# Kernel tuning notes

Measured on AMD Instinct MI355X. Metric: run time of the kernel, lower is better.

The kernel has to match this reference:

```python
import jax, jax.numpy as jnp
import numpy as np

N_NODES = 50000
HEADS = 4
OUT_DIM = 64
NEG_SLOPE = 0.2
BETA = 0.5
C_CONST = 1.0
EPS = 1e-16


def setup_inputs() -> dict:
    key = jax.random.key(0)
    ks = jax.random.split(key, 6)
    in_dim = 128
    x = jax.random.normal(ks[0], (N_NODES, in_dim), dtype=jnp.float32)
    edge_index = jax.random.randint(ks[1], (2, 800000), 0, N_NODES, dtype=jnp.int64)
    # GATConv params (glorot-ish scale)
    W = jax.random.normal(ks[2], (in_dim, HEADS * OUT_DIM), dtype=jnp.float32) * (1.0 / np.sqrt(in_dim))
    att_src = jax.random.normal(ks[3], (HEADS, OUT_DIM), dtype=jnp.float32) * (1.0 / np.sqrt(OUT_DIM))
    att_dst = jax.random.normal(ks[4], (HEADS, OUT_DIM), dtype=jnp.float32) * (1.0 / np.sqrt(OUT_DIM))
    bias = jnp.zeros((HEADS * OUT_DIM,), dtype=jnp.float32)
    return {"x": x, "edge_index": edge_index, "W": W, "att_src": att_src,
            "att_dst": att_dst, "bias": bias}


def _gat_conv(x, edge_index, W, att_src, att_dst, bias):
    N = x.shape[0]
    # add self loops (PyG GATConv default)
    loop = jnp.arange(N, dtype=edge_index.dtype)
    src = jnp.concatenate([edge_index[0], loop])
    dst = jnp.concatenate([edge_index[1], loop])
    # linear transform: [N, H, F]
    h = (x @ W).reshape(N, HEADS, OUT_DIM)
    # per-node attention logits: [N, H]
    a_src = jnp.einsum('nhf,hf->nh', h, att_src)
    a_dst = jnp.einsum('nhf,hf->nh', h, att_dst)
    # per-edge logits and segment softmax over destination nodes
    e = jax.nn.leaky_relu(a_src[src] + a_dst[dst], negative_slope=NEG_SLOPE)  # [E, H]
    m = jax.ops.segment_max(e, dst, num_segments=N)                           # [N, H]
    ex = jnp.exp(e - m[dst])
    s = jax.ops.segment_sum(ex, dst, num_segments=N)                          # [N, H]
    alpha = ex / (s[dst] + EPS)                                               # [E, H]
    # aggregate messages: [N, H, F]
    out = jax.ops.segment_sum(alpha[:, :, None] * h[src], dst, num_segments=N)
    return out.reshape(N, HEADS * OUT_DIM) + bias


def reference(x, edge_index, W, att_src, att_dst, bias):
    # eval mode: feature dropout and attention dropout are identity
    z = _gat_conv(x, edge_index, W, att_src, att_dst, bias)
    return BETA * z + (C_CONST - BETA) * jax.nn.elu(z)
```

## Files before the change

### kernel.cpp

```cpp
#include <hip/hip_runtime.h>
#include <hip/hip_bf16.h>

typedef unsigned short u16;
typedef __attribute__((ext_vector_type(8))) short bf16x8;
typedef __attribute__((ext_vector_type(4))) float f32x4;

#define HEADS 4
#define OUT_DIM 64
#define HF 256
#define IN_DIM 128
#define NEG_SLOPE 0.2f
#define EPSF 1e-16f

__device__ __forceinline__ float braw2f(u16 u) {
    union { float f; unsigned int i; } c; c.i = ((unsigned int)u) << 16; return c.f;
}
__device__ __forceinline__ u16 f2braw(float v) {
    __hip_bfloat16 t = __float2bfloat16(v);
    return *(u16*)&t;
}
__device__ __forceinline__ float lrelu(float e) { return e < 0.f ? NEG_SLOPE * e : e; }

__device__ __forceinline__ bool detect_i64(const int* ei) {
    return (ei[1] | ei[3] | ei[5] | ei[7] | ei[9] | ei[11] | ei[13] | ei[15]) == 0;
}
__device__ __forceinline__ void get_edge(const int* ei, int E, int t, bool i64,
                                         int& s, int& d) {
    if (t < E) {
        if (i64) { s = ei[2 * t]; d = ei[2 * (E + t)]; }
        else     { s = ei[t];     d = ei[E + t]; }
    } else {
        s = d = t - E;
    }
}

__global__ __launch_bounds__(256) void init_kernel(const float* __restrict__ W,
                                                   const float* __restrict__ att_s,
                                                   const float* __restrict__ att_d,
                                                   float* __restrict__ wa_s,
                                                   float* __restrict__ wa_d,
                                                   int* __restrict__ cnt, int N, int NZ) {
    int b = blockIdx.x;
    if (b < NZ) {
        int i = b * 256 + threadIdx.x;
        if (i < N) cnt[i] = 0;
    } else {
        for (int idx = threadIdx.x; idx < HEADS * IN_DIM; idx += 256) {
            int h = idx >> 7, k = idx & 127;
            float ss = 0.f, sd = 0.f;
            for (int f = 0; f < OUT_DIM; ++f) {
                float wv = W[k * HF + h * OUT_DIM + f];
                ss = fmaf(wv, att_s[h * OUT_DIM + f], ss);
                sd = fmaf(wv, att_d[h * OUT_DIM + f], sd);
            }
            wa_s[idx] = ss;
            wa_d[idx] = sd;
        }
    }
}

__global__ __launch_bounds__(256) void phase1_kernel(const float* __restrict__ x,
                                                     const int* __restrict__ ei,
                                                     const float* __restrict__ W,
                                                     const float* __restrict__ wa_s,
                                                     const float* __restrict__ wa_d,
                                                     float* __restrict__ a_src,
                                                     float* __restrict__ a_dst,
                                                     u16* __restrict__ xb,
                                                     u16* __restrict__ Wfrag,
                                                     int* __restrict__ cnt,
                                                     int N, int E, int NA, int NC) {
    int b = blockIdx.x;
    if (b < NA) {
        int v = (b * 256 + threadIdx.x) >> 6;
        int l = threadIdx.x & 63;
        if (v >= N) return;
        int h = l >> 4, c = l & 15, kc = c * 8;

        const float4* xr = (const float4*)(x + (size_t)v * IN_DIM + kc);
        float4 x0 = xr[0], x1 = xr[1];
        const float4* s4 = (const float4*)(wa_s + h * IN_DIM + kc);
        const float4* d4 = (const float4*)(wa_d + h * IN_DIM + kc);
        float4 s0 = s4[0], s1 = s4[1], d0 = d4[0], d1 = d4[1];

        float ps = x0.x*s0.x + x0.y*s0.y + x0.z*s0.z + x0.w*s0.w
                 + x1.x*s1.x + x1.y*s1.y + x1.z*s1.z + x1.w*s1.w;
        float pd = x0.x*d0.x + x0.y*d0.y + x0.z*d0.z + x0.w*d0.w
                 + x1.x*d1.x + x1.y*d1.y + x1.z*d1.z + x1.w*d1.w;
        #pragma unroll
        for (int off = 1; off < 16; off <<= 1) {
            ps += __shfl_xor(ps, off);
            pd += __shfl_xor(pd, off);
        }
        if (c == 0) {
            a_src[v * HEADS + h] = ps;
            a_dst[v * HEADS + h] = pd;
        }
        if (h == 0) {
            uint4 u;
            u.x = (unsigned)f2braw(x0.x) | ((unsigned)f2braw(x0.y) << 16);
            u.y = (unsigned)f2braw(x0.z) | ((unsigned)f2braw(x0.w) << 16);
            u.z = (unsigned)f2braw(x1.x) | ((unsigned)f2braw(x1.y) << 16);
            u.w = (unsigned)f2braw(x1.z) | ((unsigned)f2braw(x1.w) << 16);
            *(uint4*)(xb + (size_t)v * IN_DIM + kc) = u;
        }
    } else if (b < NA + NC) {
        int t = (b - NA) * 256 + threadIdx.x;
        if (t >= E + N) return;
        bool i64 = detect_i64(ei);
        int src, dst; get_edge(ei, E, t, i64, src, dst);
        if (src >= 0 && src < N && dst >= 0 && dst < N) atomicAdd(cnt + dst, 1);
    } else {
        int bb = b - NA - NC;
        for (int idx = bb * 256 + threadIdx.x; idx < 32768; idx += 8 * 256) {
            int j = idx & 7, l = (idx >> 3) & 63, t = (idx >> 9) & 3;
            int s = (idx >> 11) & 3, h = (idx >> 13) & 3;
            int k = s * 32 + ((l >> 4) & 3) * 8 + j;
            int col = h * OUT_DIM + t * 16 + (l & 15);
            Wfrag[idx] = f2braw(W[k * HF + col]);
        }
    }
}

__global__ __launch_bounds__(256) void scan1_kernel(const int* __restrict__ cnt,
                                                    int* __restrict__ indptr,
                                                    int* __restrict__ bsum, int N) {
    __shared__ int sc[256];
    int tid = threadIdx.x;
    int idx = blockIdx.x * 256 + tid;
    int v = (idx < N) ? cnt[idx] : 0;
    sc[tid] = v;
    __syncthreads();
    #pragma unroll
    for (int off = 1; off < 256; off <<= 1) {
        int t = (tid >= off) ? sc[tid - off] : 0;
        __syncthreads();
        sc[tid] += t;
        __syncthreads();
    }
    if (idx < N) indptr[idx + 1] = sc[tid];
    if (tid == 255) bsum[blockIdx.x] = sc[255];
}

__global__ __launch_bounds__(1024) void scan2_kernel(int* __restrict__ bsum, int T) {
    __shared__ int sc[1024];
    int tid = threadIdx.x;
    int v = (tid < T) ? bsum[tid] : 0;
    sc[tid] = v;
    __syncthreads();
    #pragma unroll
    for (int off = 1; off < 1024; off <<= 1) {
        int t = (tid >= off) ? sc[tid - off] : 0;
        __syncthreads();
        sc[tid] += t;
        __syncthreads();
    }
    if (tid < T) bsum[tid] = sc[tid] - v;
}

__global__ __launch_bounds__(256) void scan3_kernel(int* __restrict__ indptr,
                                                    const int* __restrict__ bsum,
                                                    int* __restrict__ cnt, int N) {
    int idx = blockIdx.x * 256 + threadIdx.x;
    if (idx < N) {
        indptr[idx + 1] += bsum[blockIdx.x];
        cnt[idx] = 0;
    }
    if (idx == 0) indptr[0] = 0;
}

__global__ __launch_bounds__(256) void fill_kernel(const int* __restrict__ ei,
                                                   const int* __restrict__ indptr,
                                                   int* __restrict__ cur,
                                                   int* __restrict__ slots,
                                                   uint2* __restrict__ wslots,
                                                   const float* __restrict__ a_src,
                                                   const float* __restrict__ a_dst,
                                                   int E, int N) {
    int t = blockIdx.x * 256 + threadIdx.x;
    if (t >= E + N) return;
    bool i64 = detect_i64(ei);
    int src, dst; get_edge(ei, E, t, i64, src, dst);
    if (src >= 0 && src < N && dst >= 0 && dst < N) {
        int pos = atomicAdd(cur + dst, 1);
        int idx = indptr[dst] + pos;
        slots[idx] = src;
        if (wslots) {
            float4 as = ((const float4*)a_src)[src];
            float4 ad = ((const float4*)a_dst)[dst];
            float w0 = __expf(lrelu(as.x + ad.x));
            float w1 = __expf(lrelu(as.y + ad.y));
            float w2 = __expf(lrelu(as.z + ad.z));
            float w3 = __expf(lrelu(as.w + ad.w));
            uint2 wp;
            wp.x = (unsigned)f2braw(w0) | ((unsigned)f2braw(w1) << 16);
            wp.y = (unsigned)f2braw(w2) | ((unsigned)f2braw(w3) << 16);
            wslots[idx] = wp;
        }
    }
}

__global__ __launch_bounds__(512) void gather_w_kernel(const int* __restrict__ indptr,
                                                       const int* __restrict__ slots,
                                                       const uint2* __restrict__ wslots,
                                                       const u16* __restrict__ xb,
                                                       u16* __restrict__ Gout, int N, int ET) {
    int l = threadIdx.x & 63;
    int gw = blockIdx.x * 8 + (threadIdx.x >> 6);
    int v = gw * 4 + (l >> 4);
    if (v >= N) return;
    int c = l & 15, kc = c * 8;

    int beg = indptr[v], end = indptr[v + 1];
    beg = max(0, min(beg, ET));
    end = max(beg, min(end, ET));

    float ls0 = 0.f, ls1 = 0.f, ls2 = 0.f, ls3 = 0.f;
    float G0[8] = {0,0,0,0,0,0,0,0};
    float G1[8] = {0,0,0,0,0,0,0,0};
    float G2[8] = {0,0,0,0,0,0,0,0};
    float G3[8] = {0,0,0,0,0,0,0,0};

    int j = beg;
    for (; j + 2 <= end; j += 2) {
        int s0 = max(0, min(slots[j],     N - 1));
        int s1 = max(0, min(slots[j + 1], N - 1));
        uint2 wp0 = wslots[j];
        uint2 wp1 = wslots[j + 1];
        uint4 r0 = *(const uint4*)(xb + (size_t)s0 * IN_DIM + kc);
        uint4 r1 = *(const uint4*)(xb + (size_t)s1 * IN_DIM + kc);

        float a0 = braw2f(wp0.x & 0xffff), a1 = braw2f(wp0.x >> 16);
        float a2 = braw2f(wp0.y & 0xffff), a3 = braw2f(wp0.y >> 16);
        ls0 += a0; ls1 += a1; ls2 += a2; ls3 += a3;
        {
            float xv[8];
            xv[0] = braw2f(r0.x & 0xffff); xv[1] = braw2f(r0.x >> 16);
            xv[2] = braw2f(r0.y & 0xffff); xv[3] = braw2f(r0.y >> 16);
            xv[4] = braw2f(r0.z & 0xffff); xv[5] = braw2f(r0.z >> 16);
            xv[6] = braw2f(r0.w & 0xffff); xv[7] = braw2f(r0.w >> 16);
            #pragma unroll
            for (int q = 0; q < 8; ++q) {
                G0[q] = fmaf(a0, xv[q], G0[q]);
                G1[q] = fmaf(a1, xv[q], G1[q]);
                G2[q] = fmaf(a2, xv[q], G2[q]);
                G3[q] = fmaf(a3, xv[q], G3[q]);
            }
        }
        float b0 = braw2f(wp1.x & 0xffff), b1 = braw2f(wp1.x >> 16);
        float b2 = braw2f(wp1.y & 0xffff), b3 = braw2f(wp1.y >> 16);
        ls0 += b0; ls1 += b1; ls2 += b2; ls3 += b3;
        {
            float xv[8];
            xv[0] = braw2f(r1.x & 0xffff); xv[1] = braw2f(r1.x >> 16);
            xv[2] = braw2f(r1.y & 0xffff); xv[3] = braw2f(r1.y >> 16);
            xv[4] = braw2f(r1.z & 0xffff); xv[5] = braw2f(r1.z >> 16);
            xv[6] = braw2f(r1.w & 0xffff); xv[7] = braw2f(r1.w >> 16);
            #pragma unroll
            for (int q = 0; q < 8; ++q) {
                G0[q] = fmaf(b0, xv[q], G0[q]);
                G1[q] = fmaf(b1, xv[q], G1[q]);
                G2[q] = fmaf(b2, xv[q], G2[q]);
                G3[q] = fmaf(b3, xv[q], G3[q]);
            }
        }
    }
    if (j < end) {
        int s0 = max(0, min(slots[j], N - 1));
        uint2 wp0 = wslots[j];
        uint4 r0 = *(const uint4*)(xb + (size_t)s0 * IN_DIM + kc);
        float a0 = braw2f(wp0.x & 0xffff), a1 = braw2f(wp0.x >> 16);
        float a2 = braw2f(wp0.y & 0xffff), a3 = braw2f(wp0.y >> 16);
        ls0 += a0; ls1 += a1; ls2 += a2; ls3 += a3;
        float xv[8];
        xv[0] = braw2f(r0.x & 0xffff); xv[1] = braw2f(r0.x >> 16);
        xv[2] = braw2f(r0.y & 0xffff); xv[3] = braw2f(r0.y >> 16);
        xv[4] = braw2f(r0.z & 0xffff); xv[5] = braw2f(r0.z >> 16);
        xv[6] = braw2f(r0.w & 0xffff); xv[7] = braw2f(r0.w >> 16);
        #pragma unroll
        for (int q = 0; q < 8; ++q) {
            G0[q] = fmaf(a0, xv[q], G0[q]);
            G1[q] = fmaf(a1, xv[q], G1[q]);
            G2[q] = fmaf(a2, xv[q], G2[q]);
            G3[q] = fmaf(a3, xv[q], G3[q]);
        }
    }

    float i0 = 1.f / (ls0 + EPSF), i1 = 1.f / (ls1 + EPSF);
    float i2 = 1.f / (ls2 + EPSF), i3 = 1.f / (ls3 + EPSF);
    u16* gout = Gout + (size_t)v * 512 + kc;
    #pragma unroll
    for (int h = 0; h < 4; ++h) {
        const float* G = h == 0 ? G0 : h == 1 ? G1 : h == 2 ? G2 : G3;
        float inv = h == 0 ? i0 : h == 1 ? i1 : h == 2 ? i2 : i3;
        uint4 u;
        u.x = (unsigned)f2braw(G[0] * inv) | ((unsigned)f2braw(G[1] * inv) << 16);
        u.y = (unsigned)f2braw(G[2] * inv) | ((unsigned)f2braw(G[3] * inv) << 16);
        u.z = (unsigned)f2braw(G[4] * inv) | ((unsigned)f2braw(G[5] * inv) << 16);
        u.w = (unsigned)f2braw(G[6] * inv) | ((unsigned)f2braw(G[7] * inv) << 16);
        *(uint4*)(gout + h * 128) = u;
    }
}

__global__ __launch_bounds__(512) void gather_bf_kernel(const int* __restrict__ indptr,
                                                        const int* __restrict__ slots,
                                                        const u16* __restrict__ xb,
                                                        const float* __restrict__ a_src,
                                                        const float* __restrict__ a_dst,
                                                        u16* __restrict__ Gout, int N, int ET) {
    int v = (blockIdx.x * 512 + threadIdx.x) >> 6;
    int l = threadIdx.x & 63;
    if (v >= N) return;
    int h = l >> 4, c = l & 15, kc = c * 8;

    int beg = indptr[v], end = indptr[v + 1];
    beg = max(0, min(beg, ET));
    end = max(beg, min(end, ET));
    float adh = a_dst[v * HEADS + h];

    float ls = 0.f;
    float G[8] = {0.f,0.f,0.f,0.f,0.f,0.f,0.f,0.f};

    int j = beg;
    for (; j + 4 <= end; j += 4) {
        int s0 = max(0, min(slots[j],     N - 1));
        int s1 = max(0, min(slots[j + 1], N - 1));
        int s2 = max(0, min(slots[j + 2], N - 1));
        int s3 = max(0, min(slots[j + 3], N - 1));
        float w0 = __expf(lrelu(a_src[s0 * HEADS + h] + adh));
        float w1 = __expf(lrelu(a_src[s1 * HEADS + h] + adh));
        float w2 = __expf(lrelu(a_src[s2 * HEADS + h] + adh));
        float w3 = __expf(lrelu(a_src[s3 * HEADS + h] + adh));
        uint4 r0 = *(const uint4*)(xb + (size_t)s0 * IN_DIM + kc);
        uint4 r1 = *(const uint4*)(xb + (size_t)s1 * IN_DIM + kc);
        uint4 r2 = *(const uint4*)(xb + (size_t)s2 * IN_DIM + kc);
        uint4 r3 = *(const uint4*)(xb + (size_t)s3 * IN_DIM + kc);
        ls += (w0 + w1) + (w2 + w3);
        unsigned ua[4];
        ua[0]=r0.x; ua[1]=r0.y; ua[2]=r0.z; ua[3]=r0.w;
        #pragma unroll
        for (int q = 0; q < 4; ++q) {
            G[2*q]   = fmaf(w0, braw2f(ua[q] & 0xffff), G[2*q]);
            G[2*q+1] = fmaf(w0, braw2f(ua[q] >> 16),    G[2*q+1]);
        }
        ua[0]=r1.x; ua[1]=r1.y; ua[2]=r1.z; ua[3]=r1.w;
        #pragma unroll
        for (int q = 0; q < 4; ++q) {
            G[2*q]   = fmaf(w1, braw2f(ua[q] & 0xffff), G[2*q]);
            G[2*q+1] = fmaf(w1, braw2f(ua[q] >> 16),    G[2*q+1]);
        }
        ua[0]=r2.x; ua[1]=r2.y; ua[2]=r2.z; ua[3]=r2.w;
        #pragma unroll
        for (int q = 0; q < 4; ++q) {
            G[2*q]   = fmaf(w2, braw2f(ua[q] & 0xffff), G[2*q]);
            G[2*q+1] = fmaf(w2, braw2f(ua[q] >> 16),    G[2*q+1]);
        }
        ua[0]=r3.x; ua[1]=r3.y; ua[2]=r3.z; ua[3]=r3.w;
        #pragma unroll
        for (int q = 0; q < 4; ++q) {
            G[2*q]   = fmaf(w3, braw2f(ua[q] & 0xffff), G[2*q]);
            G[2*q+1] = fmaf(w3, braw2f(ua[q] >> 16),    G[2*q+1]);
        }
    }
    for (; j < end; ++j) {
        int s0 = max(0, min(slots[j], N - 1));
        float w0 = __expf(lrelu(a_src[s0 * HEADS + h] + adh));
        uint4 r0 = *(const uint4*)(xb + (size_t)s0 * IN_DIM + kc);
        ls += w0;
        unsigned ua[4]; ua[0]=r0.x; ua[1]=r0.y; ua[2]=r0.z; ua[3]=r0.w;
        #pragma unroll
        for (int q = 0; q < 4; ++q) {
            G[2*q]   = fmaf(w0, braw2f(ua[q] & 0xffff), G[2*q]);
            G[2*q+1] = fmaf(w0, braw2f(ua[q] >> 16),    G[2*q+1]);
        }
    }

    float inv = 1.f / (ls + EPSF);
    uint4 u;
    u.x = (unsigned)f2braw(G[0] * inv) | ((unsigned)f2braw(G[1] * inv) << 16);
    u.y = (unsigned)f2braw(G[2] * inv) | ((unsigned)f2braw(G[3] * inv) << 16);
    u.z = (unsigned)f2braw(G[4] * inv) | ((unsigned)f2braw(G[5] * inv) << 16);
    u.w = (unsigned)f2braw(G[6] * inv) | ((unsigned)f2braw(G[7] * inv) << 16);
    *(uint4*)(Gout + (size_t)v * 512 + h * 128 + kc) = u;
}

__global__ __launch_bounds__(512) void gather_f32_kernel(const int* __restrict__ indptr,
                                                         const int* __restrict__ slots,
                                                         const float* __restrict__ x,
                                                         const float* __restrict__ a_src,
                                                         const float* __restrict__ a_dst,
                                                         u16* __restrict__ Gout, int N, int ET) {
    int v = (blockIdx.x * 512 + threadIdx.x) >> 6;
    int l = threadIdx.x & 63;
    if (v >= N) return;
    int h = l >> 4, c = l & 15, kc = c * 8;

    int beg = indptr[v], end = indptr[v + 1];
    beg = max(0, min(beg, ET));
    end = max(beg, min(end, ET));
    float adh = a_dst[v * HEADS + h];

    float ls = 0.f;
    float G[8] = {0.f,0.f,0.f,0.f,0.f,0.f,0.f,0.f};
    for (int j = beg; j < end; ++j) {
        int s0 = max(0, min(slots[j], N - 1));
        float w0 = __expf(lrelu(a_src[s0 * HEADS + h] + adh));
        const float4* xr0 = (const float4*)(x + (size_t)s0 * IN_DIM + kc);
        float4 a0 = xr0[0], b0 = xr0[1];
        ls += w0;
        G[0]=fmaf(w0,a0.x,G[0]); G[1]=fmaf(w0,a0.y,G[1]);
        G[2]=fmaf(w0,a0.z,G[2]); G[3]=fmaf(w0,a0.w,G[3]);
        G[4]=fmaf(w0,b0.x,G[4]); G[5]=fmaf(w0,b0.y,G[5]);
        G[6]=fmaf(w0,b0.z,G[6]); G[7]=fmaf(w0,b0.w,G[7]);
    }
    float inv = 1.f / (ls + EPSF);
    uint4 u;
    u.x = (unsigned)f2braw(G[0] * inv) | ((unsigned)f2braw(G[1] * inv) << 16);
    u.y = (unsigned)f2braw(G[2] * inv) | ((unsigned)f2braw(G[3] * inv) << 16);
    u.z = (unsigned)f2braw(G[4] * inv) | ((unsigned)f2braw(G[5] * inv) << 16);
    u.w = (unsigned)f2braw(G[6] * inv) | ((unsigned)f2braw(G[7] * inv) << 16);
    *(uint4*)(Gout + (size_t)v * 512 + h * 128 + kc) = u;
}

__global__ __launch_bounds__(256) void zgemm_kernel(const u16* __restrict__ Wfrag,
                                                    const float* __restrict__ bias,
                                                    float* __restrict__ out, int N) {
    int h = threadIdx.x >> 6;
    int l = threadIdx.x & 63;
    int q = l >> 4, mcol = l & 15;
    int nb = blockIdx.x * 16;

    const u16* G = (const u16*)out;
    bool valid = (nb + mcol) < N;
    int vA = valid ? nb + mcol : N - 1;
    const u16* gp = G + (size_t)vA * 512 + h * 128 + q * 8;
    bf16x8 A[4];
    A[0] = *(const bf16x8*)(gp);
    A[1] = *(const bf16x8*)(gp + 32);
    A[2] = *(const bf16x8*)(gp + 64);
    A[3] = *(const bf16x8*)(gp + 96);
    if (!valid) {
        bf16x8 zz = {0,0,0,0,0,0,0,0};
        A[0] = zz; A[1] = zz; A[2] = zz; A[3] = zz;
    }

    f32x4 acc0 = {0.f,0.f,0.f,0.f}, acc1 = acc0, acc2 = acc0, acc3 = acc0;
    #pragma unroll
    for (int s = 0; s < 4; ++s) {
        const u16* wb = Wfrag + (((h * 4 + s) * 4) << 9) + l * 8;
        bf16x8 B0 = *(const bf16x8*)(wb);
        bf16x8 B1 = *(const bf16x8*)(wb + 512);
        bf16x8 B2 = *(const bf16x8*)(wb + 1024);
        bf16x8 B3 = *(const bf16x8*)(wb + 1536);
        acc0 = __builtin_amdgcn_mfma_f32_16x16x32_bf16(A[s], B0, acc0, 0, 0, 0);
        acc1 = __builtin_amdgcn_mfma_f32_16x16x32_bf16(A[s], B1, acc1, 0, 0, 0);
        acc2 = __builtin_amdgcn_mfma_f32_16x16x32_bf16(A[s], B2, acc2, 0, 0, 0);
        acc3 = __builtin_amdgcn_mfma_f32_16x16x32_bf16(A[s], B3, acc3, 0, 0, 0);
    }

    #pragma unroll
    for (int t = 0; t < 4; ++t) {
        f32x4 a = t == 0 ? acc0 : t == 1 ? acc1 : t == 2 ? acc2 : acc3;
        float b = bias[h * OUT_DIM + t * 16 + mcol];
        #pragma unroll
        for (int r = 0; r < 4; ++r) {
            int v = nb + q * 4 + r;
            if (v < N) {
                float z = a[r] + b;
                float y = z > 0.f ? z : 0.5f * z + 0.5f * (__expf(z) - 1.f);
                out[(size_t)v * HF + h * OUT_DIM + t * 16 + mcol] = y;
            }
        }
    }
}

extern "C" void kernel_launch(void* const* d_in, const int* in_sizes, int n_in,
                              void* d_out, int out_size, void* d_ws, size_t ws_size,
                              hipStream_t stream) {
    const float* x       = (const float*)d_in[0];
    const int*   ei      = (const int*)d_in[1];
    const float* W       = (const float*)d_in[2];
    const float* att_src = (const float*)d_in[3];
    const float* att_dst = (const float*)d_in[4];
    const float* bias    = (const float*)d_in[5];

    const int N = in_sizes[0] / IN_DIM;
    const int E = in_sizes[1] / 2;
    const int ET = E + N;
    const int NT = (N + 255) / 256;

    char* ws = (char*)d_ws;
    size_t off = 0;
    float* wa_s   = (float*)(ws + off); off += HEADS * IN_DIM * 4;
    float* wa_d   = (float*)(ws + off); off += HEADS * IN_DIM * 4;
    u16*   Wfrag  = (u16*)(ws + off);   off += 32768 * 2;
    float* a_src  = (float*)(ws + off); off += (size_t)N * HEADS * 4;
    float* a_dst  = (float*)(ws + off); off += (size_t)N * HEADS * 4;
    int*   indptr = (int*)(ws + off);   off += ((size_t)(N + 1) * 4 + 15) & ~(size_t)15;
    int*   cnt    = (int*)(ws + off);   off += ((size_t)N * 4 + 15) & ~(size_t)15;
    int*   bsum   = (int*)(ws + off);   off += 1024 * 4;
    int*   slots  = (int*)(ws + off);   off += ((size_t)ET * 4 + 15) & ~(size_t)15;
    u16*   xb     = (u16*)(ws + off);   size_t need_bf = off + (size_t)N * IN_DIM * 2;
    uint2* wslots = (uint2*)(ws + need_bf);
    size_t need_w = need_bf + (size_t)ET * 8;
    bool use_bf = (ws_size >= need_bf);
    bool use_w  = (ws_size >= need_w);

    const int NA = (N + 3) / 4;
    const int NC = (ET + 255) / 256;

    init_kernel<<<NT + 1, 256, 0, stream>>>(W, att_src, att_dst, wa_s, wa_d, cnt, N, NT);
    phase1_kernel<<<NA + NC + 8, 256, 0, stream>>>(x, ei, W, wa_s, wa_d, a_src, a_dst,
                                                   use_bf ? xb : (u16*)d_out,
                                                   Wfrag, cnt, N, E, NA, NC);
    scan1_kernel<<<NT, 256, 0, stream>>>(cnt, indptr, bsum, N);
    scan2_kernel<<<1, 1024, 0, stream>>>(bsum, NT);
    scan3_kernel<<<NT, 256, 0, stream>>>(indptr, bsum, cnt, N);
    fill_kernel<<<(ET + 255) / 256, 256, 0, stream>>>(ei, indptr, cnt, slots,
                                                      use_w ? wslots : (uint2*)0,
                                                      a_src, a_dst, E, N);
    if (use_w) {
        int nwaves = (N + 3) / 4;
        gather_w_kernel<<<(nwaves * 64 + 511) / 512, 512, 0, stream>>>(indptr, slots,
                                                                       wslots, xb,
                                                                       (u16*)d_out, N, ET);
    } else if (use_bf) {
        gather_bf_kernel<<<(N * 64 + 511) / 512, 512, 0, stream>>>(indptr, slots, xb,
                                                                   a_src, a_dst,
                                                                   (u16*)d_out, N, ET);
    } else {
        gather_f32_kernel<<<(N * 64 + 511) / 512, 512, 0, stream>>>(indptr, slots, x,
                                                                    a_src, a_dst,
                                                                    (u16*)d_out, N, ET);
    }
    zgemm_kernel<<<(N + 15) / 16, 256, 0, stream>>>(Wfrag, bias, (float*)d_out, N);
}
```

Measured before the change: 267.3 us.

## Replace three-kernel prefix scan with atomic wave-level offset allocation

Swaps the scan1/scan2/scan3 exclusive scan for a single kernel. Each wave does a shuffle scan of in-degrees and reserves a contiguous slot range with one atomicAdd on a global counter. The gather kernels now read the offset and degree instead of indptr[v], indptr[v+1], and a separate cur array is zeroed in init, which removes two kernel launches and their dependency chain. The phase1 node path is also reworked so each 16-lane group handles one node across all four heads, cutting redundant x loads and writing a_src/a_dst as float4; the cost is that CSR segments are no longer stored in node order.

```diff
diff --git a/kernel.cpp b/kernel.cpp
--- a/kernel.cpp
+++ b/kernel.cpp
@@ -39,11 +39,15 @@
                                                    const float* __restrict__ att_d,
                                                    float* __restrict__ wa_s,
                                                    float* __restrict__ wa_d,
-                                                   int* __restrict__ cnt, int N, int NZ) {
+                                                   int* __restrict__ cnt,
+                                                   int* __restrict__ cur,
+                                                   int* __restrict__ gcnt,
+                                                   int N, int NZ) {
     int b = blockIdx.x;
+    if (b == 0 && threadIdx.x == 0) *gcnt = 0;
     if (b < NZ) {
         int i = b * 256 + threadIdx.x;
-        if (i < N) cnt[i] = 0;
+        if (i < N) { cnt[i] = 0; cur[i] = 0; }
     } else {
         for (int idx = threadIdx.x; idx < HEADS * IN_DIM; idx += 256) {
             int h = idx >> 7, k = idx & 127;
@@ -72,37 +76,47 @@
                                                      int N, int E, int NA, int NC) {
     int b = blockIdx.x;
     if (b < NA) {
-        int v = (b * 256 + threadIdx.x) >> 6;
+        int wid = threadIdx.x >> 6;
         int l = threadIdx.x & 63;
+        int g = l >> 4, c = l & 15, kc = c * 8;
+        int v = b * 16 + wid * 4 + g;
         if (v >= N) return;
-        int h = l >> 4, c = l & 15, kc = c * 8;
 
         const float4* xr = (const float4*)(x + (size_t)v * IN_DIM + kc);
         float4 x0 = xr[0], x1 = xr[1];
-        const float4* s4 = (const float4*)(wa_s + h * IN_DIM + kc);
-        const float4* d4 = (const float4*)(wa_d + h * IN_DIM + kc);
-        float4 s0 = s4[0], s1 = s4[1], d0 = d4[0], d1 = d4[1];
-
-        float ps = x0.x*s0.x + x0.y*s0.y + x0.z*s0.z + x0.w*s0.w
-                 + x1.x*s1.x + x1.y*s1.y + x1.z*s1.z + x1.w*s1.w;
-        float pd = x0.x*d0.x + x0.y*d0.y + x0.z*d0.z + x0.w*d0.w
-                 + x1.x*d1.x + x1.y*d1.y + x1.z*d1.z + x1.w*d1.w;
+
+        uint4 u;
+        u.x = (unsigned)f2braw(x0.x) | ((unsigned)f2braw(x0.y) << 16);
+        u.y = (unsigned)f2braw(x0.z) | ((unsigned)f2braw(x0.w) << 16);
+        u.z = (unsigned)f2braw(x1.x) | ((unsigned)f2braw(x1.y) << 16);
+        u.w = (unsigned)f2braw(x1.z) | ((unsigned)f2braw(x1.w) << 16);
+        *(uint4*)(xb + (size_t)v * IN_DIM + kc) = u;
+
+        float ps[4], pd[4];
+        #pragma unroll
+        for (int h = 0; h < 4; ++h) {
+            const float4* s4 = (const float4*)(wa_s + h * IN_DIM + kc);
+            const float4* d4 = (const float4*)(wa_d + h * IN_DIM + kc);
+            float4 s0 = s4[0], s1 = s4[1], d0 = d4[0], d1 = d4[1];
+            ps[h] = x0.x*s0.x + x0.y*s0.y + x0.z*s0.z + x0.w*s0.w
+                  + x1.x*s1.x + x1.y*s1.y + x1.z*s1.z + x1.w*s1.w;
+            pd[h] = x0.x*d0.x + x0.y*d0.y + x0.z*d0.z + x0.w*d0.w
+                  + x1.x*d1.x + x1.y*d1.y + x1.z*d1.z + x1.w*d1.w;
+        }
         #pragma unroll
         for (int off = 1; off < 16; off <<= 1) {
-            ps += __shfl_xor(ps, off);
-            pd += __shfl_xor(pd, off);
+            #pragma unroll
+            for (int h = 0; h < 4; ++h) {
+                ps[h] += __shfl_xor(ps[h], off);
+                pd[h] += __shfl_xor(pd[h], off);
+            }
         }
         if (c == 0) {
-            a_src[v * HEADS + h] = ps;
-            a_dst[v * HEADS + h] = pd;
-        }
-        if (h == 0) {
-            uint4 u;
-            u.x = (unsigned)f2braw(x0.x) | ((unsigned)f2braw(x0.y) << 16);
-            u.y = (unsigned)f2braw(x0.z) | ((unsigned)f2braw(x0.w) << 16);
-            u.z = (unsigned)f2braw(x1.x) | ((unsigned)f2braw(x1.y) << 16);
-            u.w = (unsigned)f2braw(x1.z) | ((unsigned)f2braw(x1.w) << 16);
-            *(uint4*)(xb + (size_t)v * IN_DIM + kc) = u;
+            float4 vs, vd;
+            vs.x = ps[0]; vs.y = ps[1]; vs.z = ps[2]; vs.w = ps[3];
+            vd.x = pd[0]; vd.y = pd[1]; vd.z = pd[2]; vd.w = pd[3];
+            *(float4*)(a_src + (size_t)v * HEADS) = vs;
+            *(float4*)(a_dst + (size_t)v * HEADS) = vd;
         }
     } else if (b < NA + NC) {
         int t = (b - NA) * 256 + threadIdx.x;
@@ -122,55 +136,26 @@
     }
 }
 
-__global__ __launch_bounds__(256) void scan1_kernel(const int* __restrict__ cnt,
-                                                    int* __restrict__ indptr,
-                                                    int* __restrict__ bsum, int N) {
-    __shared__ int sc[256];
-    int tid = threadIdx.x;
-    int idx = blockIdx.x * 256 + tid;
-    int v = (idx < N) ? cnt[idx] : 0;
-    sc[tid] = v;
-    __syncthreads();
+__global__ __launch_bounds__(256) void offset_kernel(const int* __restrict__ cnt,
+                                                     int* __restrict__ offs,
+                                                     int* __restrict__ gcnt, int N) {
+    int idx = blockIdx.x * 256 + threadIdx.x;
+    int l = threadIdx.x & 63;
+    int d = (idx < N) ? cnt[idx] : 0;
+    int s = d;
     #pragma unroll
-    for (int off = 1; off < 256; off <<= 1) {
-        int t = (tid >= off) ? sc[tid - off] : 0;
-        __syncthreads();
-        sc[tid] += t;
-        __syncthreads();
-    }
-    if (idx < N) indptr[idx + 1] = sc[tid];
-    if (tid == 255) bsum[blockIdx.x] = sc[255];
-}
-
-__global__ __launch_bounds__(1024) void scan2_kernel(int* __restrict__ bsum, int T) {
-    __shared__ int sc[1024];
-    int tid = threadIdx.x;
-    int v = (tid < T) ? bsum[tid] : 0;
-    sc[tid] = v;
-    __syncthreads();
-    #pragma unroll
-    for (int off = 1; off < 1024; off <<= 1) {
-        int t = (tid >= off) ? sc[tid - off] : 0;
-        __syncthreads();
-        sc[tid] += t;
-        __syncthreads();
-    }
-    if (tid < T) bsum[tid] = sc[tid] - v;
-}
-
-__global__ __launch_bounds__(256) void scan3_kernel(int* __restrict__ indptr,
-                                                    const int* __restrict__ bsum,
-                                                    int* __restrict__ cnt, int N) {
-    int idx = blockIdx.x * 256 + threadIdx.x;
-    if (idx < N) {
-        indptr[idx + 1] += bsum[blockIdx.x];
-        cnt[idx] = 0;
-    }
-    if (idx == 0) indptr[0] = 0;
+    for (int off = 1; off < 64; off <<= 1) {
+        int t = __shfl_up(s, off);
+        if (l >= off) s += t;
+    }
+    int base = 0;
+    if (l == 63) base = atomicAdd(gcnt, s);
+    base = __shfl(base, 63);
+    if (idx < N) offs[idx] = base + s - d;
 }
 
 __global__ __launch_bounds__(256) void fill_kernel(const int* __restrict__ ei,
-                                                   const int* __restrict__ indptr,
+                                                   const int* __restrict__ offs,
                                                    int* __restrict__ cur,
                                                    int* __restrict__ slots,
                                                    uint2* __restrict__ wslots,
@@ -183,7 +168,7 @@
     int src, dst; get_edge(ei, E, t, i64, src, dst);
     if (src >= 0 && src < N && dst >= 0 && dst < N) {
         int pos = atomicAdd(cur + dst, 1);
-        int idx = indptr[dst] + pos;
+        int idx = offs[dst] + pos;
         slots[idx] = src;
         if (wslots) {
             float4 as = ((const float4*)a_src)[src];
@@ -200,7 +185,8 @@
     }
 }
 
-__global__ __launch_bounds__(512) void gather_w_kernel(const int* __restrict__ indptr,
+__global__ __launch_bounds__(512) void gather_w_kernel(const int* __restrict__ offs,
+                                                       const int* __restrict__ cnt,
                                                        const int* __restrict__ slots,
                                                        const uint2* __restrict__ wslots,
                                                        const u16* __restrict__ xb,
@@ -211,9 +197,10 @@
     if (v >= N) return;
     int c = l & 15, kc = c * 8;
 
-    int beg = indptr[v], end = indptr[v + 1];
+    int beg = offs[v];
+    int deg = cnt[v];
     beg = max(0, min(beg, ET));
-    end = max(beg, min(end, ET));
+    int end = max(beg, min(beg + deg, ET));
 
     float ls0 = 0.f, ls1 = 0.f, ls2 = 0.f, ls3 = 0.f;
     float G0[8] = {0,0,0,0,0,0,0,0};
@@ -302,7 +289,8 @@
     }
 }
 
-__global__ __launch_bounds__(512) void gather_bf_kernel(const int* __restrict__ indptr,
+__global__ __launch_bounds__(512) void gather_bf_kernel(const int* __restrict__ offs,
+                                                        const int* __restrict__ cnt,
                                                         const int* __restrict__ slots,
                                                         const u16* __restrict__ xb,
                                                         const float* __restrict__ a_src,
@@ -313,9 +301,10 @@
     if (v >= N) return;
     int h = l >> 4, c = l & 15, kc = c * 8;
 
-    int beg = indptr[v], end = indptr[v + 1];
+    int beg = offs[v];
+    int deg = cnt[v];
     beg = max(0, min(beg, ET));
-    end = max(beg, min(end, ET));
+    int end = max(beg, min(beg + deg, ET));
     float adh = a_dst[v * HEADS + h];
 
     float ls = 0.f;
@@ -384,7 +373,8 @@
     *(uint4*)(Gout + (size_t)v * 512 + h * 128 + kc) = u;
 }
 
-__global__ __launch_bounds__(512) void gather_f32_kernel(const int* __restrict__ indptr,
+__global__ __launch_bounds__(512) void gather_f32_kernel(const int* __restrict__ offs,
+                                                         const int* __restrict__ cnt,
                                                          const int* __restrict__ slots,
                                                          const float* __restrict__ x,
                                                          const float* __restrict__ a_src,
@@ -395,9 +385,10 @@
     if (v >= N) return;
     int h = l >> 4, c = l & 15, kc = c * 8;
 
-    int beg = indptr[v], end = indptr[v + 1];
+    int beg = offs[v];
+    int deg = cnt[v];
     beg = max(0, min(beg, ET));
-    end = max(beg, min(end, ET));
+    int end = max(beg, min(beg + deg, ET));
     float adh = a_dst[v * HEADS + h];
 
     float ls = 0.f;
@@ -496,9 +487,10 @@
     u16*   Wfrag  = (u16*)(ws + off);   off += 32768 * 2;
     float* a_src  = (float*)(ws + off); off += (size_t)N * HEADS * 4;
     float* a_dst  = (float*)(ws + off); off += (size_t)N * HEADS * 4;
-    int*   indptr = (int*)(ws + off);   off += ((size_t)(N + 1) * 4 + 15) & ~(size_t)15;
+    int*   offs   = (int*)(ws + off);   off += ((size_t)N * 4 + 15) & ~(size_t)15;
     int*   cnt    = (int*)(ws + off);   off += ((size_t)N * 4 + 15) & ~(size_t)15;
-    int*   bsum   = (int*)(ws + off);   off += 1024 * 4;
+    int*   cur    = (int*)(ws + off);   off += ((size_t)N * 4 + 15) & ~(size_t)15;
+    int*   gcnt   = (int*)(ws + off);   off += 64;
     int*   slots  = (int*)(ws + off);   off += ((size_t)ET * 4 + 15) & ~(size_t)15;
     u16*   xb     = (u16*)(ws + off);   size_t need_bf = off + (size_t)N * IN_DIM * 2;
     uint2* wslots = (uint2*)(ws + need_bf);
@@ -506,30 +498,29 @@
     bool use_bf = (ws_size >= need_bf);
     bool use_w  = (ws_size >= need_w);
 
-    const int NA = (N + 3) / 4;
+    const int NA = (N + 15) / 16;
     const int NC = (ET + 255) / 256;
 
-    init_kernel<<<NT + 1, 256, 0, stream>>>(W, att_src, att_dst, wa_s, wa_d, cnt, N, NT);
+    init_kernel<<<NT + 1, 256, 0, stream>>>(W, att_src, att_dst, wa_s, wa_d,
+                                            cnt, cur, gcnt, N, NT);
     phase1_kernel<<<NA + NC + 8, 256, 0, stream>>>(x, ei, W, wa_s, wa_d, a_src, a_dst,
                                                    use_bf ? xb : (u16*)d_out,
                                                    Wfrag, cnt, N, E, NA, NC);
-    scan1_kernel<<<NT, 256, 0, stream>>>(cnt, indptr, bsum, N);
-    scan2_kernel<<<1, 1024, 0, stream>>>(bsum, NT);
-    scan3_kernel<<<NT, 256, 0, stream>>>(indptr, bsum, cnt, N);
-    fill_kernel<<<(ET + 255) / 256, 256, 0, stream>>>(ei, indptr, cnt, slots,
+    offset_kernel<<<NT, 256, 0, stream>>>(cnt, offs, gcnt, N);
+    fill_kernel<<<(ET + 255) / 256, 256, 0, stream>>>(ei, offs, cur, slots,
                                                       use_w ? wslots : (uint2*)0,
                                                       a_src, a_dst, E, N);
     if (use_w) {
         int nwaves = (N + 3) / 4;
-        gather_w_kernel<<<(nwaves * 64 + 511) / 512, 512, 0, stream>>>(indptr, slots,
+        gather_w_kernel<<<(nwaves * 64 + 511) / 512, 512, 0, stream>>>(offs, cnt, slots,
                                                                        wslots, xb,
                                                                        (u16*)d_out, N, ET);
     } else if (use_bf) {
-        gather_bf_kernel<<<(N * 64 + 511) / 512, 512, 0, stream>>>(indptr, slots, xb,
+        gather_bf_kernel<<<(N * 64 + 511) / 512, 512, 0, stream>>>(offs, cnt, slots, xb,
                                                                    a_src, a_dst,
                                                                    (u16*)d_out, N, ET);
     } else {
-        gather_f32_kernel<<<(N * 64 + 511) / 512, 512, 0, stream>>>(indptr, slots, x,
+        gather_f32_kernel<<<(N * 64 + 511) / 512, 512, 0, stream>>>(offs, cnt, slots, x,
                                                                     a_src, a_dst,
                                                                     (u16*)d_out, N, ET);
     }
```

After: 267.7 us. No clear change (+0.2%).
